# Performance work log

Measured on AMD Instinct MI355X. Metric: run time of the kernel, lower is better.

## Reference

```python
import jax, jax.numpy as jnp
import numpy as np

N = 8192      # nodes
F = 256       # input feature dim
D_OUT = 256   # output_dim


def setup_inputs() -> dict:
    key = jax.random.key(0)
    k1, k2, k3 = jax.random.split(key, 3)
    data = jax.random.normal(k1, (1, N, F), dtype=jnp.float32)
    # dense (normalized) adjacency; the original converts dense->sparse then matmuls,
    # which is mathematically a dense adj @ data product.
    adj = jax.random.uniform(k2, (1, N, N), dtype=jnp.float32)
    kernel = jax.random.normal(k3, (F, D_OUT), dtype=jnp.float32)
    return {"data": data, "adj": adj, "kernel": kernel}


def reference(data, adj, kernel):
    # af = adj @ data  : [N, N] @ [N, F] -> [N, F]  (neighbor aggregation)
    af = jnp.matmul(adj[0], data[0])
    # dense projection: [N, F] @ [F, D_OUT] -> [N, D_OUT]
    out = jnp.matmul(af, kernel)
    # expand batch dim back and apply activation (relu)
    return jax.nn.relu(out[None, :, :])
```

## Files before the change

kernel.cpp:

```cpp
#include <hip/hip_runtime.h>
#include <stdint.h>

#define AS1 __attribute__((address_space(1)))
#define AS3 __attribute__((address_space(3)))

typedef float f32x4 __attribute__((ext_vector_type(4)));
typedef __bf16 bf16x8 __attribute__((ext_vector_type(8)));

__device__ __forceinline__ unsigned short f2bf(float f) {
    uint32_t x = __float_as_uint(f);
    x += 0x7FFFu + ((x >> 16) & 1u);
    return (unsigned short)(x >> 16);
}

__device__ __forceinline__ void gload_lds16(const void* g, void* l) {
    __builtin_amdgcn_global_load_lds((const AS1 void*)g, (AS3 void*)l, 16, 0, 0);
}

__global__ __launch_bounds__(256) void wt_kernel(const float* __restrict__ W,
                                                 unsigned short* __restrict__ WT) {
    __shared__ float tile[32][33];
    const int bf = blockIdx.x & 7;
    const int bn = blockIdx.x >> 3;
    const int t = threadIdx.x;
    const int c = t & 31, r = t >> 5;
#pragma unroll
    for (int i = 0; i < 4; ++i)
        tile[r + i * 8][c] = W[(bf * 32 + r + i * 8) * 256 + bn * 32 + c];
    __syncthreads();
#pragma unroll
    for (int i = 0; i < 4; ++i)
        WT[(bn * 32 + r + i * 8) * 256 + bf * 32 + c] = f2bf(tile[c][r + i * 8]);
}

template <int LDA, int LDB, int KSTEPS, int MODE, int KSPLIT>
__global__ __launch_bounds__(256) void gemm_kernel(const float* __restrict__ A,
                                                   const unsigned short* __restrict__ B,
                                                   float* __restrict__ Out0,
                                                   float* __restrict__ Pws) {
    __shared__ float Afp[32 * 64];
    __shared__ unsigned short Blds[256 * 64];

    const int t = threadIdx.x;
    const int w = t >> 6;
    const int l = t & 63;
    const int mtile = blockIdx.x / KSPLIT;
    const int ks = blockIdx.x % KSPLIT;
    const int m0 = mtile * 32;
    const int kbase = ks * KSTEPS * 64;

    const int rowj0 = w * 4 + (l >> 4);
    const int ca = l & 15;
    const float* gAs = A + (size_t)(m0 + rowj0) * LDA + kbase +
                       ((ca ^ (rowj0 & 7)) << 2);
    char* ldsA0 = (char*)Afp + w * 1024;
    char* ldsA1 = ldsA0 + 4096;

    const int nr_base = w * 64 + (l >> 3);
    const int c16 = l & 7;

    f32x4 acc[2][4];
#pragma unroll
    for (int i = 0; i < 2; ++i)
#pragma unroll
        for (int j = 0; j < 4; ++j) acc[i][j] = (f32x4){0.f, 0.f, 0.f, 0.f};

    for (int step = 0; step < KSTEPS; ++step) {
        const int k0 = step * 64;
        __syncthreads();
#pragma unroll
        for (int i = 0; i < 8; ++i) {
            const int nr = nr_base + i * 8;
            const unsigned short* src =
                B + (size_t)nr * LDB + kbase + k0 + ((c16 ^ (nr & 7)) << 3);
            gload_lds16(src, (char*)Blds + (w * 512 + i * 64) * 16);
        }
        gload_lds16(gAs + k0, ldsA0);
        gload_lds16(gAs + (size_t)16 * LDA + k0, ldsA1);
        __syncthreads();
#pragma unroll
        for (int kh = 0; kh < 2; ++kh) {
            bf16x8 af[2], bv[4];
#pragma unroll
            for (int im = 0; im < 2; ++im) {
                const int r = im * 16 + (l & 15);
                const int cb = kh * 8 + ((l >> 4) << 1);
                const char* base = (const char*)Afp + r * 256;
                const int sw = (r & 7) << 4;
                const f32x4 u0 = *(const f32x4*)(base + ((cb << 4) ^ sw));
                const f32x4 u1 = *(const f32x4*)(base + (((cb + 1) << 4) ^ sw));
                bf16x8 a;
                a[0] = (__bf16)u0.x; a[1] = (__bf16)u0.y;
                a[2] = (__bf16)u0.z; a[3] = (__bf16)u0.w;
                a[4] = (__bf16)u1.x; a[5] = (__bf16)u1.y;
                a[6] = (__bf16)u1.z; a[7] = (__bf16)u1.w;
                af[im] = a;
            }
            const int koffb = kh * 64 + ((l >> 4) << 4);
#pragma unroll
            for (int jn = 0; jn < 4; ++jn) {
                const int n = w * 64 + jn * 16 + (l & 15);
                bv[jn] = *(const bf16x8*)((const char*)Blds +
                                          ((n * 128 + koffb) ^ ((n & 7) << 4)));
            }
#pragma unroll
            for (int im = 0; im < 2; ++im)
#pragma unroll
                for (int jn = 0; jn < 4; ++jn)
                    acc[im][jn] = __builtin_amdgcn_mfma_f32_16x16x32_bf16(
                        af[im], bv[jn], acc[im][jn], 0, 0, 0);
        }
    }

    if (MODE == 0) {
        float* Og = (KSPLIT == 1 || ks == 0)
                        ? Out0
                        : (Pws + (size_t)(ks - 1) * (8192 * 256));
#pragma unroll
        for (int im = 0; im < 2; ++im) {
            const int row0 = m0 + im * 16 + ((l >> 4) << 2);
#pragma unroll
            for (int jn = 0; jn < 4; ++jn) {
                const int col = w * 64 + jn * 16 + (l & 15);
#pragma unroll
                for (int r = 0; r < 4; ++r) {
                    float v = acc[im][jn][r];
                    if (KSPLIT == 1) v = v > 0.f ? v : 0.f;
                    Og[(size_t)(row0 + r) * 256 + col] = v;
                }
            }
        }
    } else {
        unsigned short* dkT = (unsigned short*)Out0;
#pragma unroll
        for (int im = 0; im < 2; ++im) {
            const int mb = m0 + im * 16 + ((l >> 4) << 2);
#pragma unroll
            for (int jn = 0; jn < 4; ++jn) {
                const int n = w * 64 + jn * 16 + (l & 15);
                const uint32_t lo = (uint32_t)f2bf(acc[im][jn][0]) |
                                    ((uint32_t)f2bf(acc[im][jn][1]) << 16);
                const uint32_t hi = (uint32_t)f2bf(acc[im][jn][2]) |
                                    ((uint32_t)f2bf(acc[im][jn][3]) << 16);
                uint32_t* dst = (uint32_t*)&dkT[(size_t)n * 8192 + mb];
                dst[0] = lo;
                dst[1] = hi;
            }
        }
    }
}

template <int S>
__global__ __launch_bounds__(256) void reduce_relu_kernel(float* __restrict__ out,
                                                          const float* __restrict__ P) {
    const int i = blockIdx.x * 256 + threadIdx.x;
    f32x4 v = ((const f32x4*)out)[i];
#pragma unroll
    for (int s = 0; s < S - 1; ++s) {
        const f32x4 p = ((const f32x4*)P)[(size_t)s * 524288 + i];
        v.x += p.x; v.y += p.y; v.z += p.z; v.w += p.w;
    }
    v.x = v.x > 0.f ? v.x : 0.f;
    v.y = v.y > 0.f ? v.y : 0.f;
    v.z = v.z > 0.f ? v.z : 0.f;
    v.w = v.w > 0.f ? v.w : 0.f;
    ((f32x4*)out)[i] = v;
}

extern "C" void kernel_launch(void* const* d_in, const int* in_sizes, int n_in,
                              void* d_out, int out_size, void* d_ws, size_t ws_size,
                              hipStream_t stream) {
    const float* data = (const float*)d_in[0];
    const float* adj = (const float*)d_in[1];
    const float* Wk = (const float*)d_in[2];
    float* out = (float*)d_out;

    unsigned short* WT = (unsigned short*)d_ws;
    unsigned short* dkT = (unsigned short*)((char*)d_ws + 131072);
    float* P = (float*)((char*)d_ws + 131072 + 4194304);

    const size_t base_need = 131072 + 4194304;
    const size_t part_bytes = (size_t)8192 * 256 * 4;

    wt_kernel<<<64, 256, 0, stream>>>(Wk, WT);
    gemm_kernel<256, 256, 4, 1, 1><<<256, 256, 0, stream>>>(data, WT, (float*)dkT, nullptr);
    if (ws_size >= base_need + 3 * part_bytes) {
        gemm_kernel<8192, 8192, 32, 0, 4><<<1024, 256, 0, stream>>>(adj, dkT, out, P);
        reduce_relu_kernel<4><<<2048, 256, 0, stream>>>(out, P);
    } else if (ws_size >= base_need + part_bytes) {
        gemm_kernel<8192, 8192, 64, 0, 2><<<512, 256, 0, stream>>>(adj, dkT, out, P);
        reduce_relu_kernel<2><<<2048, 256, 0, stream>>>(out, P);
    } else {
        gemm_kernel<8192, 8192, 128, 0, 1><<<256, 256, 0, stream>>>(adj, dkT, out, nullptr);
    }
}
```

Measured before the change: 122.1 us.

## Load B fragments directly to registers in adj GEMM, drop B LDS staging

The big adj GEMM now reads the dkT operand straight from global memory into MFMA register fragments instead of staging a 32KB B tile in LDS. This cuts LDS usage and lets launch_bounds request 4 blocks per CU for higher occupancy. The small GEMM is split out and converts its A operand to bf16 before writing it to LDS. Uncoalesced per-lane 16-byte global loads of B may raise L2 traffic, and without LDS staging there is no software prefetch.

Result: slower. 162.1 us (+32.7%).

```diff
diff --git a/kernel.cpp b/kernel.cpp
--- a/kernel.cpp
+++ b/kernel.cpp
@@ -33,13 +33,102 @@
         WT[(bn * 32 + r + i * 8) * 256 + bf * 32 + c] = f2bf(tile[c][r + i * 8]);
 }
 
-template <int LDA, int LDB, int KSTEPS, int MODE, int KSPLIT>
-__global__ __launch_bounds__(256) void gemm_kernel(const float* __restrict__ A,
-                                                   const unsigned short* __restrict__ B,
-                                                   float* __restrict__ Out0,
-                                                   float* __restrict__ Pws) {
+template <int LDA, int LDB, int KSTEPS>
+__global__ __launch_bounds__(256) void gemm1_kernel(const float* __restrict__ A,
+                                                    const unsigned short* __restrict__ B,
+                                                    unsigned short* __restrict__ dkT) {
+    __shared__ unsigned short Alds[32 * 64];
+    __shared__ unsigned short Blds[256 * 64];
+
+    const int t = threadIdx.x;
+    const int w = t >> 6;
+    const int l = t & 63;
+    const int m0 = blockIdx.x * 32;
+
+    const int ar = t >> 3;
+    const int kq = t & 7;
+    const float* gA = A + (size_t)(m0 + ar) * LDA + kq * 4;
+    char* aw0 = (char*)Alds + ((ar * 128 + kq * 8) ^ ((ar & 7) << 4));
+    char* aw1 = (char*)Alds + ((ar * 128 + 64 + kq * 8) ^ ((ar & 7) << 4));
+
+    const int nr_base = w * 64 + (l >> 3);
+    const int c16 = l & 7;
+
+    f32x4 acc[2][4];
+#pragma unroll
+    for (int i = 0; i < 2; ++i)
+#pragma unroll
+        for (int j = 0; j < 4; ++j) acc[i][j] = (f32x4){0.f, 0.f, 0.f, 0.f};
+
+    for (int step = 0; step < KSTEPS; ++step) {
+        const int k0 = step * 64;
+        __syncthreads();
+#pragma unroll
+        for (int i = 0; i < 8; ++i) {
+            const int nr = nr_base + i * 8;
+            const unsigned short* src =
+                B + (size_t)nr * LDB + k0 + ((c16 ^ (nr & 7)) << 3);
+            gload_lds16(src, (char*)Blds + (w * 512 + i * 64) * 16);
+        }
+        const f32x4 v0 = *(const f32x4*)(gA + k0);
+        const f32x4 v1 = *(const f32x4*)(gA + k0 + 32);
+        uint32_t p0 = (uint32_t)f2bf(v0.x) | ((uint32_t)f2bf(v0.y) << 16);
+        uint32_t p1 = (uint32_t)f2bf(v0.z) | ((uint32_t)f2bf(v0.w) << 16);
+        uint32_t p2 = (uint32_t)f2bf(v1.x) | ((uint32_t)f2bf(v1.y) << 16);
+        uint32_t p3 = (uint32_t)f2bf(v1.z) | ((uint32_t)f2bf(v1.w) << 16);
+        ((uint32_t*)aw0)[0] = p0;
+        ((uint32_t*)aw0)[1] = p1;
+        ((uint32_t*)aw1)[0] = p2;
+        ((uint32_t*)aw1)[1] = p3;
+        __syncthreads();
+#pragma unroll
+        for (int kh = 0; kh < 2; ++kh) {
+            const int koffb = kh * 64 + ((l >> 4) << 4);
+            bf16x8 af[2], bv[4];
+#pragma unroll
+            for (int im = 0; im < 2; ++im) {
+                const int r = im * 16 + (l & 15);
+                af[im] = *(const bf16x8*)((const char*)Alds +
+                                          ((r * 128 + koffb) ^ ((r & 7) << 4)));
+            }
+#pragma unroll
+            for (int jn = 0; jn < 4; ++jn) {
+                const int n = w * 64 + jn * 16 + (l & 15);
+                bv[jn] = *(const bf16x8*)((const char*)Blds +
+                                          ((n * 128 + koffb) ^ ((n & 7) << 4)));
+            }
+#pragma unroll
+            for (int im = 0; im < 2; ++im)
+#pragma unroll
+                for (int jn = 0; jn < 4; ++jn)
+                    acc[im][jn] = __builtin_amdgcn_mfma_f32_16x16x32_bf16(
+                        af[im], bv[jn], acc[im][jn], 0, 0, 0);
+        }
+    }
+
+#pragma unroll
+    for (int im = 0; im < 2; ++im) {
+        const int mb = m0 + im * 16 + ((l >> 4) << 2);
+#pragma unroll
+        for (int jn = 0; jn < 4; ++jn) {
+            const int n = w * 64 + jn * 16 + (l & 15);
+            const uint32_t lo = (uint32_t)f2bf(acc[im][jn][0]) |
+                                ((uint32_t)f2bf(acc[im][jn][1]) << 16);
+            const uint32_t hi = (uint32_t)f2bf(acc[im][jn][2]) |
+                                ((uint32_t)f2bf(acc[im][jn][3]) << 16);
+            uint32_t* dst = (uint32_t*)&dkT[(size_t)n * 8192 + mb];
+            dst[0] = lo;
+            dst[1] = hi;
+        }
+    }
+}
+
+template <int KSTEPS, int KSPLIT>
+__global__ __launch_bounds__(256, 4) void gemm2_kernel(const float* __restrict__ A,
+                                                       const unsigned short* __restrict__ B,
+                                                       float* __restrict__ Out0,
+                                                       float* __restrict__ Pws) {
     __shared__ float Afp[32 * 64];
-    __shared__ unsigned short Blds[256 * 64];
 
     const int t = threadIdx.x;
     const int w = t >> 6;
@@ -51,13 +140,16 @@
 
     const int rowj0 = w * 4 + (l >> 4);
     const int ca = l & 15;
-    const float* gAs = A + (size_t)(m0 + rowj0) * LDA + kbase +
+    const float* gAs = A + (size_t)(m0 + rowj0) * 8192 + kbase +
                        ((ca ^ (rowj0 & 7)) << 2);
     char* ldsA0 = (char*)Afp + w * 1024;
     char* ldsA1 = ldsA0 + 4096;
 
-    const int nr_base = w * 64 + (l >> 3);
-    const int c16 = l & 7;
+    const unsigned short* rp[4];
+#pragma unroll
+    for (int jn = 0; jn < 4; ++jn)
+        rp[jn] = B + (size_t)(w * 64 + jn * 16 + (l & 15)) * 8192 + kbase +
+                 ((l >> 4) << 3);
 
     f32x4 acc[2][4];
 #pragma unroll
@@ -68,19 +160,18 @@
     for (int step = 0; step < KSTEPS; ++step) {
         const int k0 = step * 64;
         __syncthreads();
-#pragma unroll
-        for (int i = 0; i < 8; ++i) {
-            const int nr = nr_base + i * 8;
-            const unsigned short* src =
-                B + (size_t)nr * LDB + kbase + k0 + ((c16 ^ (nr & 7)) << 3);
-            gload_lds16(src, (char*)Blds + (w * 512 + i * 64) * 16);
-        }
         gload_lds16(gAs + k0, ldsA0);
-        gload_lds16(gAs + (size_t)16 * LDA + k0, ldsA1);
+        gload_lds16(gAs + (size_t)16 * 8192 + k0, ldsA1);
+        bf16x8 bfr[2][4];
+#pragma unroll
+        for (int kh = 0; kh < 2; ++kh)
+#pragma unroll
+            for (int jn = 0; jn < 4; ++jn)
+                bfr[kh][jn] = *(const bf16x8*)(rp[jn] + k0 + kh * 32);
         __syncthreads();
 #pragma unroll
         for (int kh = 0; kh < 2; ++kh) {
-            bf16x8 af[2], bv[4];
+            bf16x8 af[2];
 #pragma unroll
             for (int im = 0; im < 2; ++im) {
                 const int r = im * 16 + (l & 15);
@@ -96,55 +187,28 @@
                 a[6] = (__bf16)u1.z; a[7] = (__bf16)u1.w;
                 af[im] = a;
             }
-            const int koffb = kh * 64 + ((l >> 4) << 4);
-#pragma unroll
-            for (int jn = 0; jn < 4; ++jn) {
-                const int n = w * 64 + jn * 16 + (l & 15);
-                bv[jn] = *(const bf16x8*)((const char*)Blds +
-                                          ((n * 128 + koffb) ^ ((n & 7) << 4)));
-            }
 #pragma unroll
             for (int im = 0; im < 2; ++im)
 #pragma unroll
                 for (int jn = 0; jn < 4; ++jn)
                     acc[im][jn] = __builtin_amdgcn_mfma_f32_16x16x32_bf16(
-                        af[im], bv[jn], acc[im][jn], 0, 0, 0);
-        }
-    }
-
-    if (MODE == 0) {
-        float* Og = (KSPLIT == 1 || ks == 0)
-                        ? Out0
-                        : (Pws + (size_t)(ks - 1) * (8192 * 256));
-#pragma unroll
-        for (int im = 0; im < 2; ++im) {
-            const int row0 = m0 + im * 16 + ((l >> 4) << 2);
-#pragma unroll
-            for (int jn = 0; jn < 4; ++jn) {
-                const int col = w * 64 + jn * 16 + (l & 15);
-#pragma unroll
-                for (int r = 0; r < 4; ++r) {
-                    float v = acc[im][jn][r];
-                    if (KSPLIT == 1) v = v > 0.f ? v : 0.f;
-                    Og[(size_t)(row0 + r) * 256 + col] = v;
-                }
-            }
-        }
-    } else {
-        unsigned short* dkT = (unsigned short*)Out0;
-#pragma unroll
-        for (int im = 0; im < 2; ++im) {
-            const int mb = m0 + im * 16 + ((l >> 4) << 2);
-#pragma unroll
-            for (int jn = 0; jn < 4; ++jn) {
-                const int n = w * 64 + jn * 16 + (l & 15);
-                const uint32_t lo = (uint32_t)f2bf(acc[im][jn][0]) |
-                                    ((uint32_t)f2bf(acc[im][jn][1]) << 16);
-                const uint32_t hi = (uint32_t)f2bf(acc[im][jn][2]) |
-                                    ((uint32_t)f2bf(acc[im][jn][3]) << 16);
-                uint32_t* dst = (uint32_t*)&dkT[(size_t)n * 8192 + mb];
-                dst[0] = lo;
-                dst[1] = hi;
+                        af[im], bfr[kh][jn], acc[im][jn], 0, 0, 0);
+        }
+    }
+
+    float* Og = (KSPLIT == 1 || ks == 0) ? Out0
+                                         : (Pws + (size_t)(ks - 1) * (8192 * 256));
+#pragma unroll
+    for (int im = 0; im < 2; ++im) {
+        const int row0 = m0 + im * 16 + ((l >> 4) << 2);
+#pragma unroll
+        for (int jn = 0; jn < 4; ++jn) {
+            const int col = w * 64 + jn * 16 + (l & 15);
+#pragma unroll
+            for (int r = 0; r < 4; ++r) {
+                float v = acc[im][jn][r];
+                if (KSPLIT == 1) v = v > 0.f ? v : 0.f;
+                Og[(size_t)(row0 + r) * 256 + col] = v;
             }
         }
     }
@@ -183,14 +247,14 @@
     const size_t part_bytes = (size_t)8192 * 256 * 4;
 
     wt_kernel<<<64, 256, 0, stream>>>(Wk, WT);
-    gemm_kernel<256, 256, 4, 1, 1><<<256, 256, 0, stream>>>(data, WT, (float*)dkT, nullptr);
+    gemm1_kernel<256, 256, 4><<<256, 256, 0, stream>>>(data, WT, dkT);
     if (ws_size >= base_need + 3 * part_bytes) {
-        gemm_kernel<8192, 8192, 32, 0, 4><<<1024, 256, 0, stream>>>(adj, dkT, out, P);
+        gemm2_kernel<32, 4><<<1024, 256, 0, stream>>>(adj, dkT, out, P);
         reduce_relu_kernel<4><<<2048, 256, 0, stream>>>(out, P);
     } else if (ws_size >= base_need + part_bytes) {
-        gemm_kernel<8192, 8192, 64, 0, 2><<<512, 256, 0, stream>>>(adj, dkT, out, P);
+        gemm2_kernel<64, 2><<<512, 256, 0, stream>>>(adj, dkT, out, P);
         reduce_relu_kernel<2><<<2048, 256, 0, stream>>>(out, P);
     } else {
-        gemm_kernel<8192, 8192, 128, 0, 1><<<256, 256, 0, stream>>>(adj, dkT, out, nullptr);
-    }
-}
+        gemm2_kernel<128, 1><<<256, 256, 0, stream>>>(adj, dkT, out, nullptr);
+    }
+}
```
